# Kernel tuning notes

Hardware: AMD Instinct MI355X
Metric: run time of the kernel (lower is better)

The kernel has to match this reference:

```python
import jax, jax.numpy as jnp
import numpy as np

GROUPSIZE = 128
IN_FEATURES = 4096
OUT_FEATURES = 11008
K_BLOCKS = IN_FEATURES // GROUPSIZE  # 32
M_TOKENS = 512


def setup_inputs() -> dict:
    key = jax.random.key(0)
    k1, k2, k3, k4 = jax.random.split(key, 4)
    x = jax.random.normal(k1, (M_TOKENS, IN_FEATURES), dtype=jnp.float32)
    # packed 4-bit weights: (N, K_blocks, groupsize/2) bytes, two nibbles per byte
    qweight = jax.random.randint(k2, (OUT_FEATURES, K_BLOCKS, GROUPSIZE // 2), 0, 256, dtype=jnp.int32)
    # flat per-(n, k_block) scales, size K_blocks * N
    scales = jax.random.uniform(k3, (K_BLOCKS * OUT_FEATURES,), dtype=jnp.float32) * 0.01 + 0.001
    # flat packed zero points, size K_blocks * N / 2 bytes
    qzeros = jax.random.randint(k4, (K_BLOCKS * OUT_FEATURES // 2,), 0, 256, dtype=jnp.int32)
    return {"x": x, "qweight": qweight, "scales": scales, "qzeros": qzeros}


def _dequantize_4bit(qweight, scales, qzeros):
    # qweight: (N, Kb, gs/2) int32 bytes -> unpack low nibble first, then high
    lo = qweight & 15
    hi = (qweight >> 4) & 15
    w_int = jnp.stack([lo, hi], axis=-1).reshape(OUT_FEATURES, K_BLOCKS, GROUPSIZE)
    # qzeros: flat bytes -> interleaved nibbles -> (N, Kb)
    z = jnp.stack([qzeros & 15, (qzeros >> 4) & 15], axis=-1).reshape(OUT_FEATURES, K_BLOCKS)
    s = scales.reshape(OUT_FEATURES, K_BLOCKS)
    # (q - z) * s, blockwise
    w = (w_int - z[:, :, None]).astype(s.dtype) * s[:, :, None]
    return w.reshape(OUT_FEATURES, IN_FEATURES)  # (N, K)


def reference(x, qweight, scales, qzeros):
    fp_weight = _dequantize_4bit(qweight, scales, qzeros)  # (N, K)
    return x @ fp_weight.T  # (M, N)
```

## Files before the change

### kernel.cpp

```cpp
#include <hip/hip_runtime.h>
#include <hip/hip_fp16.h>

#define M_TOK 512
#define N_OUT 11008
#define K_IN  4096

typedef _Float16 f16x8 __attribute__((ext_vector_type(8)));
typedef _Float16 f16x2 __attribute__((ext_vector_type(2)));
typedef float    f32x4 __attribute__((ext_vector_type(4)));
typedef unsigned int u32x4 __attribute__((ext_vector_type(4)));

__global__ __launch_bounds__(256) void cvt_x_kernel(const float* __restrict__ x,
                                                    _Float16* __restrict__ xh) {
    int i = (blockIdx.x * 256 + threadIdx.x) * 8;
    float4 a = *(const float4*)(x + i);
    float4 b = *(const float4*)(x + i + 4);
    f16x8 v;
    v[0] = (_Float16)a.x; v[1] = (_Float16)a.y; v[2] = (_Float16)a.z; v[3] = (_Float16)a.w;
    v[4] = (_Float16)b.x; v[5] = (_Float16)b.y; v[6] = (_Float16)b.z; v[7] = (_Float16)b.w;
    *(f16x8*)(xh + i) = v;
}

__device__ __forceinline__ void gload_lds16(const void* g, void* l) {
    __builtin_amdgcn_global_load_lds(
        (const __attribute__((address_space(1))) void*)g,
        (__attribute__((address_space(3))) void*)l,
        16, 0, 0);
}

__device__ __forceinline__ unsigned int dq_pair(unsigned int b, f16x2 fz2, f16x2 ss2) {
    unsigned int u = (b & 15u) |
                     ((b << 12) & 0xF0000u) |
                     0x64006400u;
    f16x2 h = __builtin_bit_cast(f16x2, u);
    f16x2 w = (h - fz2) * ss2;
    return __builtin_bit_cast(unsigned int, w);
}

__global__ __launch_bounds__(256, 3)
void gemm_w4_kernel(const int* __restrict__ qw,
                    const float* __restrict__ scales,
                    const int* __restrict__ qz,
                    const _Float16* __restrict__ xh,
                    float* __restrict__ out) {
    __shared__ __align__(16) char As[2][16384];

    const int hw  = blockIdx.x;
    const int logical = (hw & 7) * 86 + (hw >> 3);
    const int mx = logical & 3;
    const int ny = logical >> 2;

    const int n0 = ny * 64;
    const int m0 = mx * 128;

    const int tid  = threadIdx.x;
    const int lane = tid & 63;
    const int wid  = tid >> 6;
    const int wm   = wid >> 1;
    const int wn   = wid & 1;
    const int r16  = lane & 15;
    const int g4   = lane >> 4;

    const char* xbytes = (const char*)xh;
    const char* asrc[4];
#pragma unroll
    for (int i = 0; i < 4; ++i) {
        int row = (tid >> 3) + i * 32;
        int cb  = (tid & 7) * 16;
        int cbl = cb ^ ((row & 7) << 4);
        asrc[i] = xbytes + (size_t)(m0 + row) * (K_IN * 2) + cbl;
    }

    unsigned aoff[4][2];
#pragma unroll
    for (int mi = 0; mi < 4; ++mi) {
        int row = wm * 64 + mi * 16 + r16;
#pragma unroll
        for (int kh = 0; kh < 2; ++kh)
            aoff[mi][kh] = row * 128 + (((kh << 6) | (g4 << 4)) ^ ((row & 7) << 4));
    }

    const int nrow0 = n0 + wn * 32 + r16;
    const int nrow1 = nrow0 + 16;
    const int4* qrow0 = (const int4*)qw + (size_t)nrow0 * 512;
    const int4* qrow1 = (const int4*)qw + (size_t)nrow1 * 512;

    float s_pf0 = scales[nrow0 * 32];
    float s_pf1 = scales[nrow1 * 32];
    int   z_pf0 = qz[nrow0 * 16] & 15;
    int   z_pf1 = qz[nrow1 * 16] & 15;

    int4 qv_cur[2][2], qv_nxt[2][2];
#pragma unroll
    for (int kh = 0; kh < 2; ++kh) {
        qv_cur[0][kh] = qrow0[kh * 4 + g4];
        qv_cur[1][kh] = qrow1[kh * 4 + g4];
    }
#pragma unroll
    for (int i = 0; i < 4; ++i)
        gload_lds16(asrc[i], &As[0][(wid * 64 + i * 256) * 16]);

    f16x2 ss2[2], fz2[2];
    {
        _Float16 sh0 = (_Float16)s_pf0, sh1 = (_Float16)s_pf1;
        _Float16 fz0 = (_Float16)(float)(1024 + z_pf0), fz1 = (_Float16)(float)(1024 + z_pf1);
        ss2[0] = (f16x2){sh0, sh0}; ss2[1] = (f16x2){sh1, sh1};
        fz2[0] = (f16x2){fz0, fz0}; fz2[1] = (f16x2){fz1, fz1};
    }

    f32x4 acc[4][2];
#pragma unroll
    for (int mi = 0; mi < 4; ++mi)
#pragma unroll
        for (int ni = 0; ni < 2; ++ni)
            acc[mi][ni] = (f32x4){0.f, 0.f, 0.f, 0.f};

    __syncthreads();

#pragma unroll 2
    for (int it = 0; it < 64; ++it) {
        const int buf = it & 1;

        if (it < 63) {
#pragma unroll
            for (int i = 0; i < 4; ++i)
                gload_lds16(asrc[i] + (it + 1) * 128, &As[buf ^ 1][(wid * 64 + i * 256) * 16]);
#pragma unroll
            for (int kh = 0; kh < 2; ++kh) {
                qv_nxt[0][kh] = qrow0[(it + 1) * 8 + kh * 4 + g4];
                qv_nxt[1][kh] = qrow1[(it + 1) * 8 + kh * 4 + g4];
            }
        }
        if (((it & 1) == 0) && (it < 62)) {
            const int g = (it >> 1) + 1;
            const int f0 = nrow0 * 32 + g, f1 = nrow1 * 32 + g;
            s_pf0 = scales[f0];
            s_pf1 = scales[f1];
            z_pf0 = (qz[f0 >> 1] >> ((f0 & 1) * 4)) & 15;
            z_pf1 = (qz[f1 >> 1] >> ((f1 & 1) * 4)) & 15;
        }

        f16x8 bf[2][2];
#pragma unroll
        for (int ni = 0; ni < 2; ++ni) {
#pragma unroll
            for (int kh = 0; kh < 2; ++kh) {
                const int4 v = qv_cur[ni][kh];
                u32x4 t;
                t.x = dq_pair((unsigned)v.x, fz2[ni], ss2[ni]);
                t.y = dq_pair((unsigned)v.y, fz2[ni], ss2[ni]);
                t.z = dq_pair((unsigned)v.z, fz2[ni], ss2[ni]);
                t.w = dq_pair((unsigned)v.w, fz2[ni], ss2[ni]);
                bf[ni][kh] = __builtin_bit_cast(f16x8, t);
            }
        }

#pragma unroll
        for (int kh = 0; kh < 2; ++kh) {
            f16x8 af[4];
#pragma unroll
            for (int mi = 0; mi < 4; ++mi)
                af[mi] = *(const f16x8*)(&As[buf][0] + aoff[mi][kh]);
#pragma unroll
            for (int mi = 0; mi < 4; ++mi)
#pragma unroll
                for (int ni = 0; ni < 2; ++ni)
                    acc[mi][ni] = __builtin_amdgcn_mfma_f32_16x16x32_f16(
                        af[mi], bf[ni][kh], acc[mi][ni], 0, 0, 0);
        }

        __syncthreads();

        if (it < 63) {
#pragma unroll
            for (int kh = 0; kh < 2; ++kh) {
                qv_cur[0][kh] = qv_nxt[0][kh];
                qv_cur[1][kh] = qv_nxt[1][kh];
            }
        }
        if (((it & 1) == 1) && (it < 63)) {
            _Float16 sh0 = (_Float16)s_pf0, sh1 = (_Float16)s_pf1;
            _Float16 fz0 = (_Float16)(float)(1024 + z_pf0), fz1 = (_Float16)(float)(1024 + z_pf1);
            ss2[0] = (f16x2){sh0, sh0}; ss2[1] = (f16x2){sh1, sh1};
            fz2[0] = (f16x2){fz0, fz0}; fz2[1] = (f16x2){fz1, fz1};
        }
    }

#pragma unroll
    for (int mi = 0; mi < 4; ++mi) {
#pragma unroll
        for (int ni = 0; ni < 2; ++ni) {
            const int col   = n0 + wn * 32 + ni * 16 + r16;
            const int rbase = m0 + wm * 64 + mi * 16 + g4 * 4;
            f32x4 v = acc[mi][ni];
#pragma unroll
            for (int r = 0; r < 4; ++r)
                out[(size_t)(rbase + r) * N_OUT + col] = v[r];
        }
    }
}

extern "C" void kernel_launch(void* const* d_in, const int* in_sizes, int n_in,
                              void* d_out, int out_size, void* d_ws, size_t ws_size,
                              hipStream_t stream) {
    const float* x  = (const float*)d_in[0];
    const int*   qw = (const int*)d_in[1];
    const float* sc = (const float*)d_in[2];
    const int*   qz = (const int*)d_in[3];
    _Float16*    xh = (_Float16*)d_ws;
    float*       out = (float*)d_out;

    cvt_x_kernel<<<dim3((M_TOK * K_IN) / (256 * 8)), 256, 0, stream>>>(x, xh);

    gemm_w4_kernel<<<dim3(688), 256, 0, stream>>>(qw, sc, qz, xh, out);
}
```

Before: 282.6 us.

## Shrink GEMM block tile to 64x64 with one 16-column strip per wave

Halves the M extent of each block tile, from 128 to 64 rows, and gives each of the four waves a 64x16 output strip instead of 64x32. This halves shared memory, raises the occupancy hint, and doubles the grid to improve load balance and latency hiding. The cost is lower register-level reuse: each A fragment read from LDS now feeds half as many MFMAs. Also, each weight tile is dequantised by twice as many blocks, which raises total global weight traffic and ALU dequant work.

```diff
diff --git a/kernel.cpp b/kernel.cpp
--- a/kernel.cpp
+++ b/kernel.cpp
@@ -37,34 +37,32 @@
     return __builtin_bit_cast(unsigned int, w);
 }
 
-__global__ __launch_bounds__(256, 3)
+__global__ __launch_bounds__(256, 5)
 void gemm_w4_kernel(const int* __restrict__ qw,
                     const float* __restrict__ scales,
                     const int* __restrict__ qz,
                     const _Float16* __restrict__ xh,
                     float* __restrict__ out) {
-    __shared__ __align__(16) char As[2][16384];
+    __shared__ __align__(16) char As[2][8192];
 
     const int hw  = blockIdx.x;
-    const int logical = (hw & 7) * 86 + (hw >> 3);
-    const int mx = logical & 3;
-    const int ny = logical >> 2;
+    const int logical = (hw & 7) * 172 + (hw >> 3);
+    const int mx = logical & 7;
+    const int ny = logical >> 3;
 
     const int n0 = ny * 64;
-    const int m0 = mx * 128;
+    const int m0 = mx * 64;
 
     const int tid  = threadIdx.x;
     const int lane = tid & 63;
-    const int wid  = tid >> 6;
-    const int wm   = wid >> 1;
-    const int wn   = wid & 1;
+    const int wn   = tid >> 6;
     const int r16  = lane & 15;
     const int g4   = lane >> 4;
 
     const char* xbytes = (const char*)xh;
-    const char* asrc[4];
+    const char* asrc[2];
 #pragma unroll
-    for (int i = 0; i < 4; ++i) {
+    for (int i = 0; i < 2; ++i) {
         int row = (tid >> 3) + i * 32;
         int cb  = (tid & 7) * 16;
         int cbl = cb ^ ((row & 7) << 4);
@@ -74,46 +72,38 @@
     unsigned aoff[4][2];
 #pragma unroll
     for (int mi = 0; mi < 4; ++mi) {
-        int row = wm * 64 + mi * 16 + r16;
+        int row = mi * 16 + r16;
 #pragma unroll
         for (int kh = 0; kh < 2; ++kh)
             aoff[mi][kh] = row * 128 + (((kh << 6) | (g4 << 4)) ^ ((row & 7) << 4));
     }
 
-    const int nrow0 = n0 + wn * 32 + r16;
-    const int nrow1 = nrow0 + 16;
-    const int4* qrow0 = (const int4*)qw + (size_t)nrow0 * 512;
-    const int4* qrow1 = (const int4*)qw + (size_t)nrow1 * 512;
+    const int nrow = n0 + wn * 16 + r16;
+    const int4* qrow = (const int4*)qw + (size_t)nrow * 512;
 
-    float s_pf0 = scales[nrow0 * 32];
-    float s_pf1 = scales[nrow1 * 32];
-    int   z_pf0 = qz[nrow0 * 16] & 15;
-    int   z_pf1 = qz[nrow1 * 16] & 15;
+    float s_pf = scales[nrow * 32];
+    int   z_pf = qz[nrow * 16] & 15;
 
-    int4 qv_cur[2][2], qv_nxt[2][2];
+    int4 qv_cur[2], qv_nxt[2];
 #pragma unroll
-    for (int kh = 0; kh < 2; ++kh) {
-        qv_cur[0][kh] = qrow0[kh * 4 + g4];
-        qv_cur[1][kh] = qrow1[kh * 4 + g4];
-    }
+    for (int kh = 0; kh < 2; ++kh)
+        qv_cur[kh] = qrow[kh * 4 + g4];
 #pragma unroll
-    for (int i = 0; i < 4; ++i)
-        gload_lds16(asrc[i], &As[0][(wid * 64 + i * 256) * 16]);
+    for (int i = 0; i < 2; ++i)
+        gload_lds16(asrc[i], &As[0][(tid + i * 256) * 16]);
 
-    f16x2 ss2[2], fz2[2];
+    f16x2 ss2, fz2;
     {
-        _Float16 sh0 = (_Float16)s_pf0, sh1 = (_Float16)s_pf1;
-        _Float16 fz0 = (_Float16)(float)(1024 + z_pf0), fz1 = (_Float16)(float)(1024 + z_pf1);
-        ss2[0] = (f16x2){sh0, sh0}; ss2[1] = (f16x2){sh1, sh1};
-        fz2[0] = (f16x2){fz0, fz0}; fz2[1] = (f16x2){fz1, fz1};
+        _Float16 sh = (_Float16)s_pf;
+        _Float16 fz = (_Float16)(float)(1024 + z_pf);
+        ss2 = (f16x2){sh, sh};
+        fz2 = (f16x2){fz, fz};
     }
 
-    f32x4 acc[4][2];
+    f32x4 acc[4];
 #pragma unroll
     for (int mi = 0; mi < 4; ++mi)
-#pragma unroll
-        for (int ni = 0; ni < 2; ++ni)
-            acc[mi][ni] = (f32x4){0.f, 0.f, 0.f, 0.f};
+        acc[mi] = (f32x4){0.f, 0.f, 0.f, 0.f};
 
     __syncthreads();
 
@@ -123,36 +113,29 @@
 
         if (it < 63) {
 #pragma unroll
-            for (int i = 0; i < 4; ++i)
-                gload_lds16(asrc[i] + (it + 1) * 128, &As[buf ^ 1][(wid * 64 + i * 256) * 16]);
+            for (int i = 0; i < 2; ++i)
+                gload_lds16(asrc[i] + (it + 1) * 128, &As[buf ^ 1][(tid + i * 256) * 16]);
 #pragma unroll
-            for (int kh = 0; kh < 2; ++kh) {
-                qv_nxt[0][kh] = qrow0[(it + 1) * 8 + kh * 4 + g4];
-                qv_nxt[1][kh] = qrow1[(it + 1) * 8 + kh * 4 + g4];
-            }
+            for (int kh = 0; kh < 2; ++kh)
+                qv_nxt[kh] = qrow[(it + 1) * 8 + kh * 4 + g4];
         }
         if (((it & 1) == 0) && (it < 62)) {
             const int g = (it >> 1) + 1;
-            const int f0 = nrow0 * 32 + g, f1 = nrow1 * 32 + g;
-            s_pf0 = scales[f0];
-            s_pf1 = scales[f1];
-            z_pf0 = (qz[f0 >> 1] >> ((f0 & 1) * 4)) & 15;
-            z_pf1 = (qz[f1 >> 1] >> ((f1 & 1) * 4)) & 15;
+            const int f = nrow * 32 + g;
+            s_pf = scales[f];
+            z_pf = (qz[f >> 1] >> ((f & 1) * 4)) & 15;
         }
 
-        f16x8 bf[2][2];
+        f16x8 bf[2];
 #pragma unroll
-        for (int ni = 0; ni < 2; ++ni) {
-#pragma unroll
-            for (int kh = 0; kh < 2; ++kh) {
-                const int4 v = qv_cur[ni][kh];
-                u32x4 t;
-                t.x = dq_pair((unsigned)v.x, fz2[ni], ss2[ni]);
-                t.y = dq_pair((unsigned)v.y, fz2[ni], ss2[ni]);
-                t.z = dq_pair((unsigned)v.z, fz2[ni], ss2[ni]);
-                t.w = dq_pair((unsigned)v.w, fz2[ni], ss2[ni]);
-                bf[ni][kh] = __builtin_bit_cast(f16x8, t);
-            }
+        for (int kh = 0; kh < 2; ++kh) {
+            const int4 v = qv_cur[kh];
+            u32x4 t;
+            t.x = dq_pair((unsigned)v.x, fz2, ss2);
+            t.y = dq_pair((unsigned)v.y, fz2, ss2);
+            t.z = dq_pair((unsigned)v.z, fz2, ss2);
+            t.w = dq_pair((unsigned)v.w, fz2, ss2);
+            bf[kh] = __builtin_bit_cast(f16x8, t);
         }
 
 #pragma unroll
@@ -163,40 +146,33 @@
                 af[mi] = *(const f16x8*)(&As[buf][0] + aoff[mi][kh]);
 #pragma unroll
             for (int mi = 0; mi < 4; ++mi)
-#pragma unroll
-                for (int ni = 0; ni < 2; ++ni)
-                    acc[mi][ni] = __builtin_amdgcn_mfma_f32_16x16x32_f16(
-                        af[mi], bf[ni][kh], acc[mi][ni], 0, 0, 0);
+                acc[mi] = __builtin_amdgcn_mfma_f32_16x16x32_f16(
+                    af[mi], bf[kh], acc[mi], 0, 0, 0);
         }
 
         __syncthreads();
 
         if (it < 63) {
 #pragma unroll
-            for (int kh = 0; kh < 2; ++kh) {
-                qv_cur[0][kh] = qv_nxt[0][kh];
-                qv_cur[1][kh] = qv_nxt[1][kh];
-            }
+            for (int kh = 0; kh < 2; ++kh)
+                qv_cur[kh] = qv_nxt[kh];
         }
         if (((it & 1) == 1) && (it < 63)) {
-            _Float16 sh0 = (_Float16)s_pf0, sh1 = (_Float16)s_pf1;
-            _Float16 fz0 = (_Float16)(float)(1024 + z_pf0), fz1 = (_Float16)(float)(1024 + z_pf1);
-            ss2[0] = (f16x2){sh0, sh0}; ss2[1] = (f16x2){sh1, sh1};
-            fz2[0] = (f16x2){fz0, fz0}; fz2[1] = (f16x2){fz1, fz1};
+            _Float16 sh = (_Float16)s_pf;
+            _Float16 fz = (_Float16)(float)(1024 + z_pf);
+            ss2 = (f16x2){sh, sh};
+            fz2 = (f16x2){fz, fz};
         }
     }
 
 #pragma unroll
     for (int mi = 0; mi < 4; ++mi) {
+        const int col   = n0 + wn * 16 + r16;
+        const int rbase = m0 + mi * 16 + g4 * 4;
+        f32x4 v = acc[mi];
 #pragma unroll
-        for (int ni = 0; ni < 2; ++ni) {
-            const int col   = n0 + wn * 32 + ni * 16 + r16;
-            const int rbase = m0 + wm * 64 + mi * 16 + g4 * 4;
-            f32x4 v = acc[mi][ni];
-#pragma unroll
-            for (int r = 0; r < 4; ++r)
-                out[(size_t)(rbase + r) * N_OUT + col] = v[r];
-        }
+        for (int r = 0; r < 4; ++r)
+            out[(size_t)(rbase + r) * N_OUT + col] = v[r];
     }
 }
 
@@ -212,5 +188,5 @@
 
     cvt_x_kernel<<<dim3((M_TOK * K_IN) / (256 * 8)), 256, 0, stream>>>(x, xh);
 
-    gemm_w4_kernel<<<dim3(688), 256, 0, stream>>>(qw, sc, qz, xh, out);
+    gemm_w4_kernel<<<dim3(1376), 256, 0, stream>>>(qw, sc, qz, xh, out);
 }
```

Result: slower. 296.5 us (+4.9%).
